# Optimization experiments

Hardware: AMD Instinct MI355X
Metric: run time of the kernel (lower is better)

Reference implementation:

```python
import jax, jax.numpy as jnp
import numpy as np
from jax import lax

T_SIZE = 8        # frames
S_SIZE = 14       # spatial grid side
N_HEAD = 16
D_MODEL = 1024
L = S_SIZE * S_SIZE          # 196 patch tokens per frame
N_BATCH = 8


def _layernorm(x, g, b):
    # torch LayerNorm subclass computes in fp32 then casts back
    x32 = x.astype(jnp.float32)
    m = x32.mean(-1, keepdims=True)
    v = x32.var(-1, keepdims=True)
    return ((x32 - m) * lax.rsqrt(v + 1e-5) * g + b).astype(x.dtype)


def _mha(x, wqkv, bqkv, wo, bo, bias):
    # x: [S, B, C] seq-first like torch MHA; bias: [n_head, S, S] or None
    S, B, C = x.shape
    hd = C // N_HEAD
    qkv = x @ wqkv.T + bqkv
    q, k, v = jnp.split(qkv, 3, axis=-1)
    def h(t):
        return t.reshape(S, B, N_HEAD, hd).transpose(1, 2, 0, 3)  # [B,H,S,hd]
    q = h(q) * (1.0 / np.sqrt(hd))
    k, v = h(k), h(v)
    scores = jnp.einsum('bhqd,bhkd->bhqk', q, k)
    if bias is not None:
        scores = scores + bias[None]  # broadcast over batch (torch repeats; same math)
    a = jax.nn.softmax(scores, axis=-1)
    o = jnp.einsum('bhqk,bhkd->bhqd', a, v).transpose(2, 0, 1, 3).reshape(S, B, C)
    return o @ wo.T + bo


def _rel_idx():
    t = jnp.arange(T_SIZE)
    idx_t = t[:, None] - t[None, :] + T_SIZE - 1          # [T,T]
    c = jnp.arange(L)
    qi, qj = c // S_SIZE, c % S_SIZE
    i_off = qi[:, None] - qi[None, :] + S_SIZE - 1
    j_off = qj[:, None] - qj[None, :] + S_SIZE - 1
    idx_s = i_off * (2 * S_SIZE - 1) + j_off              # [L,L]
    return idx_t, idx_s


def reference(x, pos_w, pos_b, ln_t_g, ln_t_b, rpb_t, wqkv_t, bqkv_t, wo_t, bo_t,
              ln1_g, ln1_b, rpb_s, wqkv_s, bqkv_s, wo_s, bo_s,
              ln2_g, ln2_b, fc_w, fc_b, proj_w, proj_b):
    T, S, H, C = T_SIZE, S_SIZE, N_HEAD, D_MODEL
    LT = L * T
    N = x.shape[1]
    idx_t, idx_s = _rel_idx()

    # depthwise 3D conv positional embedding on patch tokens (token order is (h w t))
    v = x[1:].reshape(S, S, T, N, C).transpose(3, 4, 2, 0, 1)  # [N,C,T,H,W]
    conv = lax.conv_general_dilated(
        v, pos_w, (1, 1, 1), [(1, 1), (1, 1), (1, 1)],
        dimension_numbers=('NCDHW', 'OIDHW', 'NCDHW'),
        feature_group_count=C) + pos_b[None, :, None, None, None]
    tmp = (v + conv).reshape(N, C, T, L).transpose(3, 2, 0, 1).reshape(LT, N, C)
    x = jnp.concatenate([x[:1], tmp], 0)

    # temporal attention: '(l t) n c -> t (n l) c'
    xt = x[1:].reshape(L, T, N, C).transpose(1, 2, 0, 3).reshape(T, N * L, C)
    bias_t = rpb_t[idx_t].transpose(2, 0, 1)  # [H,T,T]
    rt = _mha(_layernorm(xt, ln_t_g, ln_t_b), wqkv_t, bqkv_t, wo_t, bo_t, bias_t)
    rt = rt.reshape(T, N, L, C).transpose(2, 0, 1, 3).reshape(LT, N, C)
    xt_full = x[1:] + rt

    # spatial attention with replicated cls token: 'l (t n) c' batching
    cls = jnp.tile(x[:1], (1, T, 1))                      # [1, T*N, C], t-major
    xs = jnp.concatenate([cls, xt_full.reshape(L, T * N, C)], 0)  # [L+1, T*N, C]
    bias_s = jnp.zeros((H, L + 1, L + 1), x.dtype).at[:, 1:, 1:].set(
        rpb_s[idx_s].transpose(2, 0, 1))
    rs = _mha(_layernorm(xs, ln1_g, ln1_b), wqkv_s, bqkv_s, wo_s, bo_s, bias_s)
    cls_out = rs[0].reshape(T, N, C).mean(0, keepdims=True)       # mean over frames
    spa = rs[1:].reshape(LT, N, C)                                # 'l (t n) -> (l t) n'
    x = x + jnp.concatenate([cls_out, spa], 0)

    # MLP with QuickGELU
    h = _layernorm(x, ln2_g, ln2_b) @ fc_w.T + fc_b
    h = h * jax.nn.sigmoid(1.702 * h)
    return x + (h @ proj_w.T + proj_b)


def setup_inputs() -> dict:
    key = jax.random.key(0)
    ks = jax.random.split(key, 12)
    C = D_MODEL
    f32 = jnp.float32
    def w(k, shape, s=0.02):
        return jax.random.normal(k, shape, f32) * s
    return {
        'x': jax.random.normal(ks[0], (1 + L * T_SIZE, N_BATCH, C), f32),
        'pos_w': w(ks[1], (C, 1, 3, 3, 3)),
        'pos_b': jnp.zeros((C,), f32),
        'ln_t_g': jnp.ones((C,), f32), 'ln_t_b': jnp.zeros((C,), f32),
        'rpb_t': w(ks[2], (2 * T_SIZE - 1, N_HEAD)),
        'wqkv_t': w(ks[3], (3 * C, C)), 'bqkv_t': jnp.zeros((3 * C,), f32),
        'wo_t': w(ks[4], (C, C)), 'bo_t': jnp.zeros((C,), f32),
        'ln1_g': jnp.ones((C,), f32), 'ln1_b': jnp.zeros((C,), f32),
        'rpb_s': w(ks[5], ((2 * S_SIZE - 1) ** 2, N_HEAD)),
        'wqkv_s': w(ks[6], (3 * C, C)), 'bqkv_s': jnp.zeros((3 * C,), f32),
        'wo_s': w(ks[7], (C, C)), 'bo_s': jnp.zeros((C,), f32),
        'ln2_g': jnp.ones((C,), f32), 'ln2_b': jnp.zeros((C,), f32),
        'fc_w': w(ks[8], (4 * C, C)), 'fc_b': jnp.zeros((4 * C,), f32),
        'proj_w': w(ks[9], (C, 4 * C)), 'proj_b': jnp.zeros((C,), f32),
    }
```

## Files before the change

kernel.cpp:

```cpp
#include <hip/hip_runtime.h>
#include <stdint.h>

typedef unsigned short u16;
typedef __attribute__((ext_vector_type(8))) __bf16 bf16x8;
typedef __attribute__((ext_vector_type(4))) float f32x4;

__device__ __forceinline__ float bf2f(u16 u) {
    return __uint_as_float(((unsigned int)u) << 16);
}
__device__ __forceinline__ u16 f2bf(float f) {
    unsigned int u = __float_as_uint(f);
    u += 0x7fffu + ((u >> 16) & 1u);
    return (u16)(u >> 16);
}

__device__ __forceinline__ void gl16(const u16* g, u16* l) {
    __builtin_amdgcn_global_load_lds(
        (const __attribute__((address_space(1))) unsigned int*)(uintptr_t)g,
        (__attribute__((address_space(3))) unsigned int*)(uintptr_t)l,
        16, 0, 0);
}

__global__ __launch_bounds__(256) void cvt_bf16(const float4* __restrict__ in,
                                                ushort4* __restrict__ out, int n4) {
    int tid = blockIdx.x * 256 + threadIdx.x;
    if (tid < n4) {
        float4 v = in[tid];
        ushort4 o;
        o.x = f2bf(v.x); o.y = f2bf(v.y); o.z = f2bf(v.z); o.w = f2bf(v.w);
        out[tid] = o;
    }
}

__global__ __launch_bounds__(256) void cvt_wt(const float* __restrict__ pw,
                                              float* __restrict__ wt) {
    int tid = blockIdx.x * 256 + threadIdx.x;
    if (tid < 27648) {
        int tap = tid >> 10, c = tid & 1023;
        wt[tid] = pw[c * 27 + tap];
    }
}

__global__ __launch_bounds__(256) void posembed(const float4* __restrict__ x4,
                                                const float4* __restrict__ wt4,
                                                const float4* __restrict__ pb4,
                                                float4* __restrict__ out4) {
    int tid = blockIdx.x * 256 + threadIdx.x;
    float4 xv = x4[tid];
    int rf = tid >> 11;
    if (rf == 0) { out4[tid] = xv; return; }
    int c4 = tid & 255;
    int n = (tid >> 8) & 7;
    int r = rf - 1;
    int t = r & 7, l = r >> 3;
    int i = l / 14, j = l - i * 14;
    float4 pbv = pb4[c4];
    float a0 = xv.x + pbv.x, a1 = xv.y + pbv.y, a2 = xv.z + pbv.z, a3 = xv.w + pbv.w;
#pragma unroll
    for (int dt = 0; dt < 3; dt++) {
        int tt = t + dt - 1;
        if (tt < 0 || tt > 7) continue;
#pragma unroll
        for (int di = 0; di < 3; di++) {
            int ii = i + di - 1;
            if (ii < 0 || ii > 13) continue;
#pragma unroll
            for (int dj = 0; dj < 3; dj++) {
                int jj = j + dj - 1;
                if (jj < 0 || jj > 13) continue;
                float4 w4 = wt4[(dt * 9 + di * 3 + dj) * 256 + c4];
                float4 v = x4[(size_t)(1 + ((ii * 14 + jj) << 3) + tt) * 2048 + (n << 8) + c4];
                a0 += w4.x * v.x; a1 += w4.y * v.y; a2 += w4.z * v.z; a3 += w4.w * v.w;
            }
        }
    }
    out4[tid] = (float4){a0, a1, a2, a3};
}

__global__ __launch_bounds__(256) void ln_kernel(const float* __restrict__ resid,
                                                 const u16* __restrict__ Radd,
                                                 const float* __restrict__ g,
                                                 const float* __restrict__ bb,
                                                 u16* __restrict__ out, int mode) {
    int ro = blockIdx.x;
    int tid = threadIdx.x;
    int src, n;
    long long rarow = -1;
    if (mode == 0) {
        int t = ro / 1568, b2 = ro - t * 1568;
        n = b2 / 196;
        int l = b2 - n * 196;
        src = 1 + l * 8 + t;
    } else if (mode == 1) {
        int s = ro >> 6, u = ro & 63;
        int t = u >> 3;
        n = u & 7;
        if (s == 0) src = 0;
        else { src = 1 + (s - 1) * 8 + t; rarow = (long long)(t * 1568 + n * 196 + (s - 1)); }
    } else {
        src = ro >> 3;
        n = ro & 7;
    }
    const float* xp = resid + ((size_t)src * 8 + n) * 1024 + tid * 4;
    float4 xv = *(const float4*)xp;
    float x0 = xv.x, x1 = xv.y, x2 = xv.z, x3 = xv.w;
    if (rarow >= 0) {
        const u16* rp = Radd + rarow * 1024 + tid * 4;
        x0 += bf2f(rp[0]); x1 += bf2f(rp[1]); x2 += bf2f(rp[2]); x3 += bf2f(rp[3]);
    }
    float s1 = x0 + x1 + x2 + x3;
    float s2 = x0 * x0 + x1 * x1 + x2 * x2 + x3 * x3;
#pragma unroll
    for (int off = 32; off > 0; off >>= 1) {
        s1 += __shfl_down(s1, off);
        s2 += __shfl_down(s2, off);
    }
    __shared__ float red[8];
    int lane = tid & 63, w = tid >> 6;
    if (lane == 0) { red[w] = s1; red[4 + w] = s2; }
    __syncthreads();
    float S1 = red[0] + red[1] + red[2] + red[3];
    float S2 = red[4] + red[5] + red[6] + red[7];
    float mean = S1 * (1.f / 1024.f);
    float var = S2 * (1.f / 1024.f) - mean * mean;
    float rstd = rsqrtf(var + 1e-5f);
    int c = tid * 4;
    u16* op = out + (size_t)ro * 1024 + c;
    op[0] = f2bf((x0 - mean) * rstd * g[c + 0] + bb[c + 0]);
    op[1] = f2bf((x1 - mean) * rstd * g[c + 1] + bb[c + 1]);
    op[2] = f2bf((x2 - mean) * rstd * g[c + 2] + bb[c + 2]);
    op[3] = f2bf((x3 - mean) * rstd * g[c + 3] + bb[c + 3]);
}

__global__ __launch_bounds__(256) void gemm_bf16(const u16* __restrict__ A,
                                                 const u16* __restrict__ W,
                                                 const float* __restrict__ bias,
                                                 u16* __restrict__ Co,
                                                 int M, int N, int K, int gelu,
                                                 int nx) {
    __shared__ u16 As[2][128 * 32];
    __shared__ u16 Bs[2][128 * 32];
    int tid = threadIdx.x;
    int T = gridDim.x;
    int bid = blockIdx.x;
    int w_ = (bid & 7) * (T >> 3) + (bid >> 3);
    int n0 = (w_ % nx) * 128;
    int m0 = (w_ / nx) * 128;
    int lane = tid & 63, wid = tid >> 6;
    int wm = (wid >> 1) * 64, wn = (wid & 1) * 64;
    int lm = lane & 15, q = lane >> 4;

    f32x4 acc[4][4];
#pragma unroll
    for (int i = 0; i < 4; i++)
#pragma unroll
        for (int j = 0; j < 4; j++) acc[i][j] = (f32x4){0.f, 0.f, 0.f, 0.f};

    int r0 = wid * 32 + (lane >> 2);
    int colb = (lane & 3) * 8;
    int mA0 = m0 + r0;          if (mA0 > M - 1) mA0 = M - 1;
    int mA1 = m0 + r0 + 16;     if (mA1 > M - 1) mA1 = M - 1;
    const u16* gA0 = A + (size_t)mA0 * K + colb;
    const u16* gA1 = A + (size_t)mA1 * K + colb;
    const u16* gB0 = W + (size_t)(n0 + r0) * K + colb;
    const u16* gB1 = W + (size_t)(n0 + r0 + 16) * K + colb;
    int wo = wid * 1024;

    auto loadt = [&](int b) {
        gl16(gA0, &As[b][wo]); gl16(gA1, &As[b][wo + 512]);
        gl16(gB0, &Bs[b][wo]); gl16(gB1, &Bs[b][wo + 512]);
        gA0 += 32; gA1 += 32; gB0 += 32; gB1 += 32;
    };
    auto comput = [&](int b) {
        bf16x8 af[4], bfr[4];
#pragma unroll
        for (int i = 0; i < 4; i++) af[i] = *(const bf16x8*)&As[b][(wm + i * 16 + lm) * 32 + q * 8];
#pragma unroll
        for (int j = 0; j < 4; j++) bfr[j] = *(const bf16x8*)&Bs[b][(wn + j * 16 + lm) * 32 + q * 8];
#pragma unroll
        for (int i = 0; i < 4; i++)
#pragma unroll
            for (int j = 0; j < 4; j++)
                acc[i][j] = __builtin_amdgcn_mfma_f32_16x16x32_bf16(af[i], bfr[j], acc[i][j], 0, 0, 0);
    };

    int Tt = K >> 5;
    loadt(0);
    __syncthreads();
    loadt(1); comput(0); __syncthreads();
    for (int t = 2; t + 1 < Tt; t += 2) {
        loadt(0); comput(1); __syncthreads();
        loadt(1); comput(0); __syncthreads();
    }
    comput(1);

#pragma unroll
    for (int i = 0; i < 4; i++) {
        int row_b = m0 + wm + i * 16 + q * 4;
#pragma unroll
        for (int j = 0; j < 4; j++) {
            int col = n0 + wn + j * 16 + lm;
            float bv = bias[col];
#pragma unroll
            for (int r = 0; r < 4; r++) {
                int row = row_b + r;
                if (row < M) {
                    float v = acc[i][j][r] + bv;
                    if (gelu) v = v / (1.f + __expf(-1.702f * v));
                    Co[(size_t)row * N + col] = f2bf(v);
                }
            }
        }
    }
}

__global__ __launch_bounds__(64) void attn_t(const u16* __restrict__ qkv,
                                             const float* __restrict__ rpb,
                                             u16* __restrict__ out) {
    int blk = blockIdx.x;
    int b = blk % 1568, h = blk / 1568;
    int d = threadIdx.x;
    __shared__ float qs[8][65], ks[8][65], vs[8][65];
    __shared__ float ps[8][9];
#pragma unroll
    for (int t = 0; t < 8; t++) {
        size_t row = (size_t)(t * 1568 + b) * 3072 + h * 64 + d;
        qs[t][d] = bf2f(qkv[row]) * 0.125f;
        ks[t][d] = bf2f(qkv[row + 1024]);
        vs[t][d] = bf2f(qkv[row + 2048]);
    }
    __syncthreads();
    int tq = d >> 3, tk = d & 7;
    float s = rpb[(tq - tk + 7) * 16 + h];
#pragma unroll
    for (int dd = 0; dd < 64; dd++) s += qs[tq][dd] * ks[tk][dd];
    float mx = s;
    mx = fmaxf(mx, __shfl_xor(mx, 1));
    mx = fmaxf(mx, __shfl_xor(mx, 2));
    mx = fmaxf(mx, __shfl_xor(mx, 4));
    float p = __expf(s - mx);
    float su = p;
    su += __shfl_xor(su, 1);
    su += __shfl_xor(su, 2);
    su += __shfl_xor(su, 4);
    ps[tq][tk] = p / su;
    __syncthreads();
#pragma unroll
    for (int t2 = 0; t2 < 8; t2++) {
        float o = 0.f;
#pragma unroll
        for (int k2 = 0; k2 < 8; k2++) o += ps[t2][k2] * vs[k2][d];
        out[(size_t)(t2 * 1568 + b) * 1024 + h * 64 + d] = f2bf(o);
    }
}

#define KLS 72
#define PVS 232
__global__ __launch_bounds__(256) void attn_s(const u16* __restrict__ qkv,
                                              const float* __restrict__ rpb,
                                              u16* __restrict__ out) {
    __shared__ u16 Kl[208 * KLS];
    __shared__ u16 Vt[64 * PVS];
    __shared__ u16 Pl[4][16 * PVS];
    __shared__ float rpb_l[736];
    int blk = blockIdx.x;
    int u = blk & 63, h = blk >> 6;
    int tid = threadIdx.x;
    int w = tid >> 6, lane = tid & 63;
    int lm = lane & 15, quad = lane >> 4;

    for (int idx = tid; idx < 197 * 8; idx += 256) {
        int s = idx >> 3, c8 = idx & 7;
        const u16* gp = qkv + (size_t)(s * 64 + u) * 3072 + h * 64 + c8 * 8;
        uint4 kv = *(const uint4*)(gp + 1024);
        uint4 vv = *(const uint4*)(gp + 2048);
        *(uint4*)&Kl[s * KLS + c8 * 8] = kv;
        const u16* vp = (const u16*)&vv;
#pragma unroll
        for (int j = 0; j < 8; j++) Vt[(c8 * 8 + j) * PVS + s] = vp[j];
    }
    for (int i = tid; i < 11 * KLS; i += 256) Kl[197 * KLS + i] = 0;
    for (int i = tid; i < 64 * 35; i += 256) {
        int dd = i / 35, c = 197 + (i - dd * 35);
        Vt[dd * PVS + c] = 0;
    }
    {
        for (int i = lane; i < 256; i += 64) {
            int r = i >> 4, c = 208 + (i & 15);
            Pl[w][r * PVS + c] = 0;
        }
    }
    for (int i = tid; i < 729; i += 256) rpb_l[i] = rpb[i * 16 + h];
    __syncthreads();

    for (int it = 0; it < 4; it++) {
        int qt = it * 4 + w;
        bool act = qt < 13;
        f32x4 sc[13];
        float rs[4];
        if (act) {
            int qrow = qt * 16 + lm;
            int srq = qrow > 196 ? 196 : qrow;
            const u16* qp = qkv + (size_t)(srq * 64 + u) * 3072 + h * 64 + quad * 8;
            bf16x8 aq0 = *(const bf16x8*)qp;
            bf16x8 aq1 = *(const bf16x8*)(qp + 32);
            for (int kt = 0; kt < 13; kt++) {
                bf16x8 bk0 = *(const bf16x8*)&Kl[(kt * 16 + lm) * KLS + quad * 8];
                bf16x8 bk1 = *(const bf16x8*)&Kl[(kt * 16 + lm) * KLS + 32 + quad * 8];
                f32x4 s = __builtin_amdgcn_mfma_f32_16x16x32_bf16(aq0, bk0, (f32x4){0.f, 0.f, 0.f, 0.f}, 0, 0, 0);
                sc[kt] = __builtin_amdgcn_mfma_f32_16x16x32_bf16(aq1, bk1, s, 0, 0, 0);
            }
            int tk = lm;
#pragma unroll
            for (int r = 0; r < 4; r++) {
                int qr = qt * 16 + quad * 4 + r;
                int qcl = qr > 196 ? 196 : qr;
                int lq = qcl - 1;
                int qi = lq / 14, qj = lq - qi * 14;
                for (int kt = 0; kt < 13; kt++) {
                    int tkk = kt * 16 + tk;
                    float v;
                    if (tkk >= 197) v = -1e30f;
                    else {
                        v = sc[kt][r] * 0.125f;
                        if (qr >= 1 && tkk >= 1) {
                            int lk = tkk - 1;
                            int ki = lk / 14, kj = lk - ki * 14;
                            v += rpb_l[(qi - ki + 13) * 27 + (qj - kj + 13)];
                        }
                    }
                    sc[kt][r] = v;
                }
                float mx = -3e38f;
                for (int kt = 0; kt < 13; kt++) mx = fmaxf(mx, sc[kt][r]);
                mx = fmaxf(mx, __shfl_xor(mx, 1));
                mx = fmaxf(mx, __shfl_xor(mx, 2));
                mx = fmaxf(mx, __shfl_xor(mx, 4));
                mx = fmaxf(mx, __shfl_xor(mx, 8));
                float sm = 0.f;
                for (int kt = 0; kt < 13; kt++) {
                    float p = __expf(sc[kt][r] - mx);
                    sc[kt][r] = p;
                    sm += p;
                }
                sm += __shfl_xor(sm, 1);
                sm += __shfl_xor(sm, 2);
                sm += __shfl_xor(sm, 4);
                sm += __shfl_xor(sm, 8);
                rs[r] = sm;
                for (int kt = 0; kt < 13; kt++)
                    Pl[w][(quad * 4 + r) * PVS + kt * 16 + tk] = f2bf(sc[kt][r]);
            }
        }
        __syncthreads();
        if (act) {
            bf16x8 pa[7];
#pragma unroll
            for (int kc = 0; kc < 7; kc++)
                pa[kc] = *(const bf16x8*)&Pl[w][lm * PVS + kc * 32 + quad * 8];
#pragma unroll
            for (int ct = 0; ct < 4; ct++) {
                f32x4 o = (f32x4){0.f, 0.f, 0.f, 0.f};
#pragma unroll
                for (int kc = 0; kc < 7; kc++) {
                    bf16x8 vb = *(const bf16x8*)&Vt[(ct * 16 + lm) * PVS + kc * 32 + quad * 8];
                    o = __builtin_amdgcn_mfma_f32_16x16x32_bf16(pa[kc], vb, o, 0, 0, 0);
                }
#pragma unroll
                for (int r = 0; r < 4; r++) {
                    int qr = qt * 16 + quad * 4 + r;
                    if (qr < 197)
                        out[(size_t)(qr * 64 + u) * 1024 + h * 64 + ct * 16 + lm] =
                            f2bf(o[r] / rs[r]);
                }
            }
        }
        __syncthreads();
    }
}

__global__ __launch_bounds__(256) void add_cls(const u16* __restrict__ R, float4* __restrict__ resid4) {
    int tid = blockIdx.x * 256 + threadIdx.x;
    int c4 = tid & 255, n = tid >> 8;
    float s0 = 0.f, s1 = 0.f, s2 = 0.f, s3 = 0.f;
#pragma unroll
    for (int t = 0; t < 8; t++) {
        ushort4 rv = *(const ushort4*)&R[(size_t)(t * 8 + n) * 1024 + c4 * 4];
        s0 += bf2f(rv.x); s1 += bf2f(rv.y); s2 += bf2f(rv.z); s3 += bf2f(rv.w);
    }
    float4 v = resid4[tid];
    v.x += s0 * 0.125f; v.y += s1 * 0.125f; v.z += s2 * 0.125f; v.w += s3 * 0.125f;
    resid4[tid] = v;
}

__global__ __launch_bounds__(256) void add_spa(const u16* __restrict__ R, float4* __restrict__ resid4) {
    int tid = blockIdx.x * 256 + threadIdx.x;
    int c4 = tid & 255;
    int n = (tid >> 8) & 7;
    int r = tid >> 11;
    int t = r & 7, l = r >> 3;
    int srow = (l + 1) * 64 + t * 8 + n;
    ushort4 rv = *(const ushort4*)&R[(size_t)srow * 1024 + c4 * 4];
    float4 v = resid4[tid + 2048];
    v.x += bf2f(rv.x); v.y += bf2f(rv.y); v.z += bf2f(rv.z); v.w += bf2f(rv.w);
    resid4[tid + 2048] = v;
}

__global__ __launch_bounds__(256) void add_flat(const ushort4* __restrict__ R4, float4* __restrict__ resid4) {
    int tid = blockIdx.x * 256 + threadIdx.x;
    ushort4 rv = R4[tid];
    float4 v = resid4[tid];
    v.x += bf2f(rv.x); v.y += bf2f(rv.y); v.z += bf2f(rv.z); v.w += bf2f(rv.w);
    resid4[tid] = v;
}

extern "C" void kernel_launch(void* const* d_in, const int* in_sizes, int n_in,
                              void* d_out, int out_size, void* d_ws, size_t ws_size,
                              hipStream_t stream) {
    const float* x      = (const float*)d_in[0];
    const float* pos_w  = (const float*)d_in[1];
    const float* pos_b  = (const float*)d_in[2];
    const float* ln_t_g = (const float*)d_in[3];
    const float* ln_t_b = (const float*)d_in[4];
    const float* rpb_t  = (const float*)d_in[5];
    const float* wqkv_t = (const float*)d_in[6];
    const float* bqkv_t = (const float*)d_in[7];
    const float* wo_t   = (const float*)d_in[8];
    const float* bo_t   = (const float*)d_in[9];
    const float* ln1_g  = (const float*)d_in[10];
    const float* ln1_b  = (const float*)d_in[11];
    const float* rpb_s  = (const float*)d_in[12];
    const float* wqkv_s = (const float*)d_in[13];
    const float* bqkv_s = (const float*)d_in[14];
    const float* wo_s   = (const float*)d_in[15];
    const float* bo_s   = (const float*)d_in[16];
    const float* ln2_g  = (const float*)d_in[17];
    const float* ln2_b  = (const float*)d_in[18];
    const float* fc_w   = (const float*)d_in[19];
    const float* fc_b   = (const float*)d_in[20];
    const float* proj_w = (const float*)d_in[21];
    const float* proj_b = (const float*)d_in[22];
    float* resid = (float*)d_out;

    u16* Wq_t  = (u16*)d_ws;
    u16* Wo_t  = Wq_t + 3145728;
    u16* Wq_s  = Wo_t + 1048576;
    u16* Wo_s  = Wq_s + 3145728;
    u16* Wfc   = Wo_s + 1048576;
    u16* Wpj   = Wfc  + 4194304;
    u16* Albuf = Wpj  + 4194304;
    u16* QKV   = Albuf + 12910592;
    u16* Obuf  = QKV   + 38731776;
    u16* Rbuf  = Obuf  + 12910592;
    u16* Hbuf  = QKV;
    float* wt  = (float*)QKV;

    cvt_bf16<<<3072, 256, 0, stream>>>((const float4*)wqkv_t, (ushort4*)Wq_t, 786432);
    cvt_bf16<<<1024, 256, 0, stream>>>((const float4*)wo_t,   (ushort4*)Wo_t, 262144);
    cvt_bf16<<<3072, 256, 0, stream>>>((const float4*)wqkv_s, (ushort4*)Wq_s, 786432);
    cvt_bf16<<<1024, 256, 0, stream>>>((const float4*)wo_s,   (ushort4*)Wo_s, 262144);
    cvt_bf16<<<4096, 256, 0, stream>>>((const float4*)fc_w,   (ushort4*)Wfc,  1048576);
    cvt_bf16<<<4096, 256, 0, stream>>>((const float4*)proj_w, (ushort4*)Wpj,  1048576);
    cvt_wt<<<108, 256, 0, stream>>>(pos_w, wt);

    posembed<<<12552, 256, 0, stream>>>((const float4*)x, (const float4*)wt,
                                        (const float4*)pos_b, (float4*)resid);

    ln_kernel<<<12544, 256, 0, stream>>>(resid, nullptr, ln_t_g, ln_t_b, Albuf, 0);
    gemm_bf16<<<2352, 256, 0, stream>>>(Albuf, Wq_t, bqkv_t, QKV, 12544, 3072, 1024, 0, 24);
    attn_t<<<25088, 64, 0, stream>>>(QKV, rpb_t, Obuf);
    gemm_bf16<<<784, 256, 0, stream>>>(Obuf, Wo_t, bo_t, Rbuf, 12544, 1024, 1024, 0, 8);

    ln_kernel<<<12608, 256, 0, stream>>>(resid, Rbuf, ln1_g, ln1_b, Albuf, 1);
    gemm_bf16<<<2376, 256, 0, stream>>>(Albuf, Wq_s, bqkv_s, QKV, 12608, 3072, 1024, 0, 24);
    attn_s<<<1024, 256, 0, stream>>>(QKV, rpb_s, Obuf);
    gemm_bf16<<<792, 256, 0, stream>>>(Obuf, Wo_s, bo_s, Rbuf, 12608, 1024, 1024, 0, 8);
    add_cls<<<8, 256, 0, stream>>>(Rbuf, (float4*)resid);
    add_spa<<<12544, 256, 0, stream>>>(Rbuf, (float4*)resid);

    ln_kernel<<<12552, 256, 0, stream>>>(resid, nullptr, ln2_g, ln2_b, Albuf, 2);
    gemm_bf16<<<3168, 256, 0, stream>>>(Albuf, Wfc, fc_b, Hbuf, 12552, 4096, 1024, 1, 32);
    gemm_bf16<<<792, 256, 0, stream>>>(Hbuf, Wpj, proj_b, Rbuf, 12552, 1024, 4096, 0, 8);
    add_flat<<<12552, 256, 0, stream>>>((const ushort4*)Rbuf, (float4*)resid);
}
```

Measured before the change: 1.168 ms.

## Replace 128x128 GEMM with 256x256 8-wave pipelined GEMM using swizzled LDS

Replaces the 128x128-tile, 4-wave bf16 GEMM with a 256x256-tile, 512-thread kernel that uses a K-step of 64, an XOR-swizzled LDS layout, and fine-grained interleaving of global-to-LDS loads with MFMA quarters. Waits use explicit vmcnt/lgkmcnt, MFMA sections run at raised priority, and workgroups are remapped evenly across XCDs. The larger tiles raise arithmetic intensity and cut global traffic, and the swizzle avoids LDS bank conflicts. The cost is 128KB of LDS, so only one block fits per CU, and fewer blocks (e.g. 196/200 for the N=1024 GEMMs) can leave CUs underfilled or create tail waves.

```diff
diff --git a/kernel.cpp b/kernel.cpp
--- a/kernel.cpp
+++ b/kernel.cpp
@@ -132,86 +132,147 @@
     op[3] = f2bf((x3 - mean) * rstd * g[c + 3] + bb[c + 3]);
 }
 
-__global__ __launch_bounds__(256) void gemm_bf16(const u16* __restrict__ A,
-                                                 const u16* __restrict__ W,
-                                                 const float* __restrict__ bias,
-                                                 u16* __restrict__ Co,
-                                                 int M, int N, int K, int gelu,
-                                                 int nx) {
-    __shared__ u16 As[2][128 * 32];
-    __shared__ u16 Bs[2][128 * 32];
+__global__ __launch_bounds__(512) void gemm256(const u16* __restrict__ A,
+                                               const u16* __restrict__ W,
+                                               const float* __restrict__ bias,
+                                               u16* __restrict__ Co,
+                                               int M, int N, int K, int gelu,
+                                               int nnt) {
+    __shared__ __align__(16) u16 sA[2][16384];
+    __shared__ __align__(16) u16 sB[2][16384];
     int tid = threadIdx.x;
-    int T = gridDim.x;
-    int bid = blockIdx.x;
-    int w_ = (bid & 7) * (T >> 3) + (bid >> 3);
-    int n0 = (w_ % nx) * 128;
-    int m0 = (w_ / nx) * 128;
-    int lane = tid & 63, wid = tid >> 6;
-    int wm = (wid >> 1) * 64, wn = (wid & 1) * 64;
+    int wid = tid >> 6, lane = tid & 63;
+    int wr = wid >> 2, wc = wid & 3;
     int lm = lane & 15, q = lane >> 4;
 
-    f32x4 acc[4][4];
-#pragma unroll
-    for (int i = 0; i < 4; i++)
+    int nwg = gridDim.x, orig = blockIdx.x;
+    int qq = nwg >> 3, rr = nwg & 7, xcd = orig & 7, blk = orig >> 3;
+    int wg = (xcd < rr ? xcd * (qq + 1) : rr * (qq + 1) + (xcd - rr) * qq) + blk;
+    int n0 = (wg % nnt) * 256, m0 = (wg / nnt) * 256;
+
+    int NT = K >> 6, NTm1 = NT - 1;
+
+    int rl = wid * 8 + (lane >> 3);
+    int cl = ((lane & 7) ^ (rl & 7)) * 8;
+    const u16* pA[4];
+    const u16* pB[4];
+#pragma unroll
+    for (int h2 = 0; h2 < 4; h2++) {
+        int ra = m0 + h2 * 64 + rl; if (ra > M - 1) ra = M - 1;
+        int rb = n0 + h2 * 64 + rl; if (rb > N - 1) rb = N - 1;
+        pA[h2] = A + (size_t)ra * K + cl;
+        pB[h2] = W + (size_t)rb * K + cl;
+    }
+    int ldst = wid * 512;
+
+    f32x4 acc[8][4];
+#pragma unroll
+    for (int i = 0; i < 8; i++)
 #pragma unroll
         for (int j = 0; j < 4; j++) acc[i][j] = (f32x4){0.f, 0.f, 0.f, 0.f};
 
-    int r0 = wid * 32 + (lane >> 2);
-    int colb = (lane & 3) * 8;
-    int mA0 = m0 + r0;          if (mA0 > M - 1) mA0 = M - 1;
-    int mA1 = m0 + r0 + 16;     if (mA1 > M - 1) mA1 = M - 1;
-    const u16* gA0 = A + (size_t)mA0 * K + colb;
-    const u16* gA1 = A + (size_t)mA1 * K + colb;
-    const u16* gB0 = W + (size_t)(n0 + r0) * K + colb;
-    const u16* gB1 = W + (size_t)(n0 + r0 + 16) * K + colb;
-    int wo = wid * 1024;
-
-    auto loadt = [&](int b) {
-        gl16(gA0, &As[b][wo]); gl16(gA1, &As[b][wo + 512]);
-        gl16(gB0, &Bs[b][wo]); gl16(gB1, &Bs[b][wo + 512]);
-        gA0 += 32; gA1 += 32; gB0 += 32; gB1 += 32;
-    };
-    auto comput = [&](int b) {
-        bf16x8 af[4], bfr[4];
-#pragma unroll
-        for (int i = 0; i < 4; i++) af[i] = *(const bf16x8*)&As[b][(wm + i * 16 + lm) * 32 + q * 8];
-#pragma unroll
-        for (int j = 0; j < 4; j++) bfr[j] = *(const bf16x8*)&Bs[b][(wn + j * 16 + lm) * 32 + q * 8];
-#pragma unroll
-        for (int i = 0; i < 4; i++)
-#pragma unroll
-            for (int j = 0; j < 4; j++)
-                acc[i][j] = __builtin_amdgcn_mfma_f32_16x16x32_bf16(af[i], bfr[j], acc[i][j], 0, 0, 0);
-    };
-
-    int Tt = K >> 5;
-    loadt(0);
-    __syncthreads();
-    loadt(1); comput(0); __syncthreads();
-    for (int t = 2; t + 1 < Tt; t += 2) {
-        loadt(0); comput(1); __syncthreads();
-        loadt(1); comput(0); __syncthreads();
-    }
-    comput(1);
-
-#pragma unroll
-    for (int i = 0; i < 4; i++) {
-        int row_b = m0 + wm + i * 16 + q * 4;
-#pragma unroll
-        for (int j = 0; j < 4; j++) {
-            int col = n0 + wn + j * 16 + lm;
-            float bv = bias[col];
-#pragma unroll
-            for (int r = 0; r < 4; r++) {
-                int row = row_b + r;
-                if (row < M) {
-                    float v = acc[i][j][r] + bv;
-                    if (gelu) v = v / (1.f + __expf(-1.702f * v));
-                    Co[(size_t)row * N + col] = f2bf(v);
+    bf16x8 af[4][2];
+    bf16x8 bfv[4][2];
+
+#define STG(P, D, b, h, kt) do { \
+        int _k = (kt); if (_k > NTm1) _k = NTm1; \
+        gl16(P[(h) * 2] + (size_t)_k * 64, &D[b][(h) * 8192 + ldst]); \
+        gl16(P[(h) * 2 + 1] + (size_t)_k * 64, &D[b][(h) * 8192 + 4096 + ldst]); \
+    } while (0)
+#define LDA_(b, ih) do { \
+        _Pragma("unroll") for (int iq = 0; iq < 4; iq++) \
+        _Pragma("unroll") for (int kk = 0; kk < 2; kk++) \
+            af[iq][kk] = *(const bf16x8*)&sA[b][((ih) * 128 + wr * 64 + iq * 16 + lm) * 64 + \
+                                                (((q + kk * 4) ^ (lm & 7)) * 8)]; \
+    } while (0)
+#define LDB_(b, jh) do { \
+        _Pragma("unroll") for (int jq = 0; jq < 2; jq++) \
+        _Pragma("unroll") for (int kk = 0; kk < 2; kk++) \
+            bfv[(jh) * 2 + jq][kk] = *(const bf16x8*)&sB[b][((jh) * 128 + wc * 32 + jq * 16 + lm) * 64 + \
+                                                            (((q + kk * 4) ^ (lm & 7)) * 8)]; \
+    } while (0)
+#define MMA_(ih, jh) do { \
+        __builtin_amdgcn_s_setprio(1); \
+        _Pragma("unroll") for (int iq = 0; iq < 4; iq++) \
+        _Pragma("unroll") for (int jq = 0; jq < 2; jq++) \
+        _Pragma("unroll") for (int kk = 0; kk < 2; kk++) \
+            acc[(ih) * 4 + iq][(jh) * 2 + jq] = __builtin_amdgcn_mfma_f32_16x16x32_bf16( \
+                af[iq][kk], bfv[(jh) * 2 + jq][kk], acc[(ih) * 4 + iq][(jh) * 2 + jq], 0, 0, 0); \
+        __builtin_amdgcn_s_setprio(0); \
+    } while (0)
+#define BAR __builtin_amdgcn_s_barrier()
+#define LGKM0 asm volatile("s_waitcnt lgkmcnt(0)" ::: "memory")
+#define VM6 asm volatile("s_waitcnt vmcnt(6)" ::: "memory")
+
+    STG(pA, sA, 0, 0, 0);
+    STG(pA, sA, 0, 1, 0);
+    STG(pB, sB, 0, 0, 0);
+    STG(pB, sB, 0, 1, 0);
+    STG(pA, sA, 1, 0, 1);
+    STG(pB, sB, 1, 1, 1);
+    STG(pA, sA, 1, 1, 1);
+    VM6;
+    BAR;
+
+    int S = NT >> 1;
+    for (int s = 0; s < S; s++) {
+        int t = s * 2;
+        LDA_(0, 0); LDB_(0, 0);
+        STG(pB, sB, 1, 0, t + 1);
+        BAR; LGKM0; MMA_(0, 0); BAR;
+        LDB_(0, 1);
+        STG(pA, sA, 0, 0, t + 2);
+        BAR; LGKM0; MMA_(0, 1); BAR;
+        LDA_(0, 1);
+        STG(pB, sB, 0, 1, t + 2);
+        BAR; LGKM0; MMA_(1, 1); BAR;
+        STG(pA, sA, 0, 1, t + 2);
+        VM6;
+        BAR; MMA_(1, 0); BAR;
+        LDA_(1, 0); LDB_(1, 0);
+        STG(pB, sB, 0, 0, t + 2);
+        BAR; LGKM0; MMA_(0, 0); BAR;
+        LDB_(1, 1);
+        STG(pA, sA, 1, 0, t + 3);
+        BAR; LGKM0; MMA_(0, 1); BAR;
+        LDA_(1, 1);
+        STG(pB, sB, 1, 1, t + 3);
+        BAR; LGKM0; MMA_(1, 1); BAR;
+        STG(pA, sA, 1, 1, t + 3);
+        VM6;
+        BAR; MMA_(1, 0); BAR;
+    }
+    asm volatile("s_waitcnt vmcnt(0)" ::: "memory");
+
+#pragma unroll
+    for (int ih = 0; ih < 2; ih++)
+#pragma unroll
+        for (int iq = 0; iq < 4; iq++) {
+            int row_b = m0 + ih * 128 + wr * 64 + iq * 16 + q * 4;
+#pragma unroll
+            for (int jh = 0; jh < 2; jh++)
+#pragma unroll
+                for (int jq = 0; jq < 2; jq++) {
+                    int col = n0 + jh * 128 + wc * 32 + jq * 16 + lm;
+                    float bv = bias[col];
+#pragma unroll
+                    for (int r = 0; r < 4; r++) {
+                        int row = row_b + r;
+                        if (row < M) {
+                            float v = acc[ih * 4 + iq][jh * 2 + jq][r] + bv;
+                            if (gelu) v = v / (1.f + __expf(-1.702f * v));
+                            Co[(size_t)row * N + col] = f2bf(v);
+                        }
+                    }
                 }
-            }
         }
-    }
+#undef STG
+#undef LDA_
+#undef LDB_
+#undef MMA_
+#undef BAR
+#undef LGKM0
+#undef VM6
 }
 
 __global__ __launch_bounds__(64) void attn_t(const u16* __restrict__ qkv,
@@ -467,19 +528,19 @@
                                         (const float4*)pos_b, (float4*)resid);
 
     ln_kernel<<<12544, 256, 0, stream>>>(resid, nullptr, ln_t_g, ln_t_b, Albuf, 0);
-    gemm_bf16<<<2352, 256, 0, stream>>>(Albuf, Wq_t, bqkv_t, QKV, 12544, 3072, 1024, 0, 24);
+    gemm256<<<588, 512, 0, stream>>>(Albuf, Wq_t, bqkv_t, QKV, 12544, 3072, 1024, 0, 12);
     attn_t<<<25088, 64, 0, stream>>>(QKV, rpb_t, Obuf);
-    gemm_bf16<<<784, 256, 0, stream>>>(Obuf, Wo_t, bo_t, Rbuf, 12544, 1024, 1024, 0, 8);
+    gemm256<<<196, 512, 0, stream>>>(Obuf, Wo_t, bo_t, Rbuf, 12544, 1024, 1024, 0, 4);
 
     ln_kernel<<<12608, 256, 0, stream>>>(resid, Rbuf, ln1_g, ln1_b, Albuf, 1);
-    gemm_bf16<<<2376, 256, 0, stream>>>(Albuf, Wq_s, bqkv_s, QKV, 12608, 3072, 1024, 0, 24);
+    gemm256<<<600, 512, 0, stream>>>(Albuf, Wq_s, bqkv_s, QKV, 12608, 3072, 1024, 0, 12);
     attn_s<<<1024, 256, 0, stream>>>(QKV, rpb_s, Obuf);
-    gemm_bf16<<<792, 256, 0, stream>>>(Obuf, Wo_s, bo_s, Rbuf, 12608, 1024, 1024, 0, 8);
+    gemm256<<<200, 512, 0, stream>>>(Obuf, Wo_s, bo_s, Rbuf, 12608, 1024, 1024, 0, 4);
     add_cls<<<8, 256, 0, stream>>>(Rbuf, (float4*)resid);
     add_spa<<<12544, 256, 0, stream>>>(Rbuf, (float4*)resid);
 
     ln_kernel<<<12552, 256, 0, stream>>>(resid, nullptr, ln2_g, ln2_b, Albuf, 2);
-    gemm_bf16<<<3168, 256, 0, stream>>>(Albuf, Wfc, fc_b, Hbuf, 12552, 4096, 1024, 1, 32);
-    gemm_bf16<<<792, 256, 0, stream>>>(Hbuf, Wpj, proj_b, Rbuf, 12552, 1024, 4096, 0, 8);
+    gemm256<<<800, 512, 0, stream>>>(Albuf, Wfc, fc_b, Hbuf, 12552, 4096, 1024, 1, 16);
+    gemm256<<<200, 512, 0, stream>>>(Hbuf, Wpj, proj_b, Rbuf, 12552, 1024, 4096, 0, 4);
     add_flat<<<12552, 256, 0, stream>>>((const ushort4*)Rbuf, (float4*)resid);
 }
```

Result: no change. 1.174 ms (+0.5%).
